# Optimization experiments

Hardware: AMD Instinct MI355X
Metric: run time of the kernel (lower is better)

Reference implementation:

```python
import jax, jax.numpy as jnp
import numpy as np

DIM = 768
N_HEADS = 12
HEAD_DIM = DIM // N_HEADS
BATCH = 2
SEQ = 4096


def setup_inputs() -> dict:
    key = jax.random.key(0)
    ks = jax.random.split(key, 9)
    s = 1.0 / np.sqrt(DIM)
    return {
        "x": jax.random.normal(ks[0], (BATCH, SEQ, DIM), dtype=jnp.float32),
        "Wq": jax.random.normal(ks[1], (DIM, DIM), dtype=jnp.float32) * s,
        "bq": jax.random.normal(ks[2], (DIM,), dtype=jnp.float32) * s,
        "Wk": jax.random.normal(ks[3], (DIM, DIM), dtype=jnp.float32) * s,
        "bk": jax.random.normal(ks[4], (DIM,), dtype=jnp.float32) * s,
        "Wv": jax.random.normal(ks[5], (DIM, DIM), dtype=jnp.float32) * s,
        "bv": jax.random.normal(ks[6], (DIM,), dtype=jnp.float32) * s,
        "Wo": jax.random.normal(ks[7], (DIM, DIM), dtype=jnp.float32) * s,
        "bo": jax.random.normal(ks[8], (DIM,), dtype=jnp.float32) * s,
    }


def reference(x, Wq, bq, Wk, bk, Wv, bv, Wo, bo):
    B, S, D = x.shape
    scale = 1.0 / np.sqrt(HEAD_DIM).astype(np.float32)
    # projections: [B,S,D] -> [B,H,S,Hd]
    def split_heads(t):
        return t.reshape(B, S, N_HEADS, HEAD_DIM).transpose(0, 2, 1, 3)
    q = split_heads(x @ Wq + bq)
    k = split_heads(x @ Wk + bk)
    v = split_heads(x @ Wv + bv)
    # full score matrix [B,H,S,S] as in the original (memory-bound)
    scores = jnp.einsum("bhqd,bhkd->bhqk", q, k) * scale
    attn = jax.nn.softmax(scores, axis=-1)
    out = jnp.einsum("bhqk,bhkd->bhqd", attn, v)
    out = out.transpose(0, 2, 1, 3).reshape(B, S, D)
    return out @ Wo + bo
```

## Files before the change

kernel.cpp:

```cpp
#include <hip/hip_runtime.h>
#include <hip/hip_bf16.h>
#include <math.h>

#define D_MODEL 768
#define NH 12
#define HD 64
#define BATCH 2
#define SEQ 4096
#define NROWS (BATCH * SEQ)

#define QSCALE 0.18033688011112042f

typedef __attribute__((ext_vector_type(8))) short short8;
typedef __attribute__((ext_vector_type(4))) short short4v;
typedef __attribute__((ext_vector_type(4))) float f32x4;
typedef __attribute__((ext_vector_type(16))) float f32x16;
typedef __attribute__((ext_vector_type(4))) unsigned int uint4v;

__device__ inline unsigned short f2bf(float f) {
    __hip_bfloat16 h = __float2bfloat16(f);
    return *reinterpret_cast<unsigned short*>(&h);
}

__device__ __forceinline__ unsigned int cvtpk_bf16(float lo, float hi) {
    unsigned int d;
    asm("v_cvt_pk_bf16_f32 %0, %1, %2" : "=v"(d) : "v"(lo), "v"(hi));
    return d;
}

__device__ __forceinline__ short8 u4_as_s8(uint4v u) {
    return *reinterpret_cast<short8*>(&u);
}

__device__ __forceinline__ void async_ld16(const unsigned short* g, unsigned short* l) {
    __builtin_amdgcn_global_load_lds(
        (const __attribute__((address_space(1))) void*)g,
        (__attribute__((address_space(3))) void*)l, 16, 0, 0);
}

__global__ __launch_bounds__(256) void convert_x_k(
    const float* __restrict__ x, unsigned short* __restrict__ xb)
{
    size_t i = ((size_t)blockIdx.x * 256 + threadIdx.x) * 8;
    float4 a = *(const float4*)(x + i);
    float4 b = *(const float4*)(x + i + 4);
    short8 o;
    o[0] = (short)f2bf(a.x); o[1] = (short)f2bf(a.y);
    o[2] = (short)f2bf(a.z); o[3] = (short)f2bf(a.w);
    o[4] = (short)f2bf(b.x); o[5] = (short)f2bf(b.y);
    o[6] = (short)f2bf(b.z); o[7] = (short)f2bf(b.w);
    *(short8*)(xb + i) = o;
}

__global__ __launch_bounds__(256) void convert_wt_k(
    const float* __restrict__ Wq, const float* __restrict__ Wk,
    const float* __restrict__ Wv, const float* __restrict__ Wo,
    unsigned short* __restrict__ wt)
{
    const float* W = (blockIdx.z == 0) ? Wq : (blockIdx.z == 1) ? Wk
                   : (blockIdx.z == 2) ? Wv : Wo;
    unsigned short* dst = wt + (size_t)blockIdx.z * D_MODEL * D_MODEL;
    __shared__ float tile[64][65];
    const int k0 = blockIdx.x * 64, n0 = blockIdx.y * 64;
    const int t = threadIdx.x;
    const int r = t >> 2, seg = t & 3;
    const float* src = W + (size_t)(k0 + r) * D_MODEL + n0 + seg * 16;
    #pragma unroll
    for (int i = 0; i < 4; ++i) {
        float4 v = *(const float4*)(src + i * 4);
        tile[r][seg * 16 + i * 4 + 0] = v.x;
        tile[r][seg * 16 + i * 4 + 1] = v.y;
        tile[r][seg * 16 + i * 4 + 2] = v.z;
        tile[r][seg * 16 + i * 4 + 3] = v.w;
    }
    __syncthreads();
    unsigned short* d = dst + (size_t)(n0 + r) * D_MODEL + k0 + seg * 16;
    short8 o0, o1;
    #pragma unroll
    for (int j = 0; j < 8; ++j) o0[j] = (short)f2bf(tile[seg * 16 + j][r]);
    #pragma unroll
    for (int j = 0; j < 8; ++j) o1[j] = (short)f2bf(tile[seg * 16 + 8 + j][r]);
    *(short8*)(d) = o0;
    *(short8*)(d + 8) = o1;
}

#define GEMM_STAGE(AS, BS, APTR, BPTR, KK)                                   \
    {                                                                        \
        _Pragma("unroll")                                                    \
        for (int j = 0; j < 4; ++j) {                                        \
            int c = (w * 4 + j) * 64 + lane;                                 \
            async_ld16(APTR + (size_t)(r0 + (c >> 3)) * D_MODEL + (KK) + (c & 7) * 8, \
                       &AS[0][0] + (size_t)c * 8);                           \
        }                                                                    \
        _Pragma("unroll")                                                    \
        for (int j = 0; j < 2; ++j) {                                        \
            int c = (w * 2 + j) * 64 + lane;                                 \
            async_ld16(BPTR + (size_t)(c0 + (c >> 3)) * D_MODEL + (KK) + (c & 7) * 8, \
                       &BS[0][0] + (size_t)c * 8);                           \
        }                                                                    \
    }

#define GEMM_COMPUTE(AS, BS)                                                 \
    {                                                                        \
        _Pragma("unroll")                                                    \
        for (int ks = 0; ks < 2; ++ks) {                                     \
            short8 af[2], bf[4];                                             \
            af[0] = *(const short8*)&AS[w * 32 + col][ks * 32 + quad * 8];   \
            af[1] = *(const short8*)&AS[w * 32 + 16 + col][ks * 32 + quad * 8]; \
            _Pragma("unroll")                                                \
            for (int nt = 0; nt < 4; ++nt)                                   \
                bf[nt] = *(const short8*)&BS[nt * 16 + col][ks * 32 + quad * 8]; \
            _Pragma("unroll")                                                \
            for (int mt = 0; mt < 2; ++mt)                                   \
                _Pragma("unroll")                                            \
                for (int nt = 0; nt < 4; ++nt)                               \
                    acc[mt][nt] = __builtin_amdgcn_mfma_f32_16x16x32_bf16(   \
                        af[mt], bf[nt], acc[mt][nt], 0, 0, 0);               \
        }                                                                    \
    }

__global__ __launch_bounds__(256) void qkv_mfma_k(
    const unsigned short* __restrict__ xb,
    const unsigned short* __restrict__ wt,
    const float* __restrict__ bq, const float* __restrict__ bk,
    const float* __restrict__ bv,
    unsigned short* __restrict__ qb,
    unsigned short* __restrict__ kb,
    unsigned short* __restrict__ vtb)
{
    __shared__ unsigned short As0[128][64], As1[128][64];
    __shared__ unsigned short Bs0[64][64],  Bs1[64][64];
    const int z = blockIdx.z;
    const unsigned short* Wt = wt + (size_t)z * D_MODEL * D_MODEL;
    const float* bias = (z == 0) ? bq : (z == 1) ? bk : bv;
    const int t = threadIdx.x;
    const int w = t >> 6, lane = t & 63, quad = lane >> 4, col = lane & 15;
    const int r0 = blockIdx.x * 128;
    const int c0 = blockIdx.y * 64;

    f32x4 acc[2][4] = {};

    GEMM_STAGE(As0, Bs0, xb, Wt, 0);
    __syncthreads();
    #pragma unroll
    for (int kp = 0; kp < 6; ++kp) {
        GEMM_STAGE(As1, Bs1, xb, Wt, kp * 128 + 64);
        GEMM_COMPUTE(As0, Bs0);
        __syncthreads();
        if (kp < 5) GEMM_STAGE(As0, Bs0, xb, Wt, kp * 128 + 128);
        GEMM_COMPUTE(As1, Bs1);
        __syncthreads();
    }

    const int h = blockIdx.y;
    #pragma unroll
    for (int nt = 0; nt < 4; ++nt) {
        const float bv_ = bias[c0 + nt * 16 + col];
        const int hd = nt * 16 + col;
        #pragma unroll
        for (int mt = 0; mt < 2; ++mt) {
            #pragma unroll
            for (int reg = 0; reg < 4; ++reg) {
                int r = r0 + w * 32 + mt * 16 + quad * 4 + reg;
                int b = r >> 12, s = r & (SEQ - 1);
                float val = acc[mt][nt][reg] + bv_;
                size_t bh = (size_t)(b * NH + h);
                if (z == 0)
                    qb[(bh * SEQ + s) * HD + hd] = f2bf(val * QSCALE);
                else if (z == 1)
                    kb[(bh * SEQ + s) * HD + hd] = f2bf(val);
                else
                    vtb[(bh * HD + hd) * SEQ + s] = f2bf(val);
            }
        }
    }
}

__global__ __launch_bounds__(256) void out_mfma_k(
    const unsigned short* __restrict__ ab,
    const unsigned short* __restrict__ wot,
    const float* __restrict__ bo,
    float* __restrict__ out)
{
    __shared__ unsigned short As0[128][64], As1[128][64];
    __shared__ unsigned short Bs0[64][64],  Bs1[64][64];
    const int t = threadIdx.x;
    const int w = t >> 6, lane = t & 63, quad = lane >> 4, col = lane & 15;
    const int r0 = blockIdx.x * 128;
    const int c0 = blockIdx.y * 64;

    f32x4 acc[2][4] = {};

    GEMM_STAGE(As0, Bs0, ab, wot, 0);
    __syncthreads();
    #pragma unroll
    for (int kp = 0; kp < 6; ++kp) {
        GEMM_STAGE(As1, Bs1, ab, wot, kp * 128 + 64);
        GEMM_COMPUTE(As0, Bs0);
        __syncthreads();
        if (kp < 5) GEMM_STAGE(As0, Bs0, ab, wot, kp * 128 + 128);
        GEMM_COMPUTE(As1, Bs1);
        __syncthreads();
    }

    #pragma unroll
    for (int nt = 0; nt < 4; ++nt) {
        const float bv_ = bo[c0 + nt * 16 + col];
        #pragma unroll
        for (int mt = 0; mt < 2; ++mt) {
            #pragma unroll
            for (int reg = 0; reg < 4; ++reg) {
                int r = r0 + w * 32 + mt * 16 + quad * 4 + reg;
                out[(size_t)r * D_MODEL + c0 + nt * 16 + col] = acc[mt][nt][reg] + bv_;
            }
        }
    }
}

__device__ __forceinline__ void softmax_pack(
    const f32x16& s, float& lsum, short8& pf0, short8& pf1)
{
    float p[16];
    #pragma unroll
    for (int r = 0; r < 16; ++r)
        p[r] = __builtin_amdgcn_exp2f(s[r]);
    lsum += (((p[0] + p[1]) + (p[2] + p[3])) + ((p[4] + p[5]) + (p[6] + p[7])))
          + (((p[8] + p[9]) + (p[10] + p[11])) + ((p[12] + p[13]) + (p[14] + p[15])));
    unsigned int c01 = cvtpk_bf16(p[0],  p[1]);
    unsigned int c45 = cvtpk_bf16(p[4],  p[5]);
    unsigned int c23 = cvtpk_bf16(p[2],  p[3]);
    unsigned int c67 = cvtpk_bf16(p[6],  p[7]);
    unsigned int c89 = cvtpk_bf16(p[8],  p[9]);
    unsigned int cCD = cvtpk_bf16(p[12], p[13]);
    unsigned int cAB = cvtpk_bf16(p[10], p[11]);
    unsigned int cEF = cvtpk_bf16(p[14], p[15]);
    auto r0 = __builtin_amdgcn_permlane32_swap((int)c01, (int)c45, false, false);
    auto r1 = __builtin_amdgcn_permlane32_swap((int)c23, (int)c67, false, false);
    auto r2 = __builtin_amdgcn_permlane32_swap((int)c89, (int)cCD, false, false);
    auto r3 = __builtin_amdgcn_permlane32_swap((int)cAB, (int)cEF, false, false);
    uint4v u0, u1;
    u0[0] = (unsigned int)r0[0]; u0[1] = (unsigned int)r1[0];
    u0[2] = (unsigned int)r0[1]; u0[3] = (unsigned int)r1[1];
    u1[0] = (unsigned int)r2[0]; u1[1] = (unsigned int)r3[0];
    u1[2] = (unsigned int)r2[1]; u1[3] = (unsigned int)r3[1];
    pf0 = u4_as_s8(u0);
    pf1 = u4_as_s8(u1);
}

__global__ __launch_bounds__(256) void flash_mfma_k(
    const unsigned short* __restrict__ qb,
    const unsigned short* __restrict__ kb,
    const unsigned short* __restrict__ vtb,
    unsigned short* __restrict__ ab)
{
    __shared__ unsigned short Ks[64][66];
    __shared__ unsigned short Vts[64][66];

    const int t = threadIdx.x;
    const int w = t >> 6, lane = t & 63;
    const int l31 = lane & 31, hi = lane >> 5;
    const int q0 = blockIdx.x * 128;
    const int h = blockIdx.y, b = blockIdx.z;
    const size_t bh = (size_t)b * NH + h;
    const unsigned short* qg = qb + bh * SEQ * HD;
    const unsigned short* kg = kb + bh * SEQ * HD;
    const unsigned short* vg = vtb + bh * HD * SEQ;

    short8 qf[4];
    {
        const unsigned short* src = qg + (size_t)(q0 + w * 32 + l31) * HD + hi * 8;
        #pragma unroll
        for (int ks = 0; ks < 4; ++ks)
            qf[ks] = *(const short8*)(src + ks * 16);
    }

    f32x16 oacc[2] = {};
    float lsum = 0.f;
    const int srow = lane, sseg = w;

    short8 kr0, kr1, vr0, vr1;
    {
        const unsigned short* kp = kg + (size_t)srow * HD + sseg * 16;
        kr0 = *(const short8*)(kp);
        kr1 = *(const short8*)(kp + 8);
        const unsigned short* vp = vg + (size_t)srow * SEQ + sseg * 16;
        vr0 = *(const short8*)(vp);
        vr1 = *(const short8*)(vp + 8);
    }

    for (int kt = 0; kt < SEQ; kt += 64) {
        __syncthreads();
        *(short8*)&Ks[srow][sseg * 16]      = kr0;
        *(short8*)&Ks[srow][sseg * 16 + 8]  = kr1;
        *(short8*)&Vts[srow][sseg * 16]     = vr0;
        *(short8*)&Vts[srow][sseg * 16 + 8] = vr1;
        if (kt + 64 < SEQ) {
            const unsigned short* kp = kg + (size_t)(kt + 64 + srow) * HD + sseg * 16;
            kr0 = *(const short8*)(kp);
            kr1 = *(const short8*)(kp + 8);
            const unsigned short* vp = vg + (size_t)srow * SEQ + kt + 64 + sseg * 16;
            vr0 = *(const short8*)(vp);
            vr1 = *(const short8*)(vp + 8);
        }
        __syncthreads();

        short8 pf[4];
        #pragma unroll
        for (int kti = 0; kti < 2; ++kti) {
            f32x16 s = {};
            __builtin_amdgcn_s_setprio(1);
            #pragma unroll
            for (int ks = 0; ks < 4; ++ks) {
                short8 kf = *(const short8*)&Ks[kti * 32 + l31][ks * 16 + hi * 8];
                s = __builtin_amdgcn_mfma_f32_32x32x16_bf16(kf, qf[ks], s, 0, 0, 0);
            }
            __builtin_amdgcn_s_setprio(0);
            softmax_pack(s, lsum, pf[kti * 2 + 0], pf[kti * 2 + 1]);
        }

        __builtin_amdgcn_s_setprio(1);
        #pragma unroll
        for (int ks = 0; ks < 4; ++ks) {
            short8 pfk = pf[ks];
            #pragma unroll
            for (int dt = 0; dt < 2; ++dt) {
                short8 vf = *(const short8*)&Vts[dt * 32 + l31][ks * 16 + hi * 8];
                oacc[dt] = __builtin_amdgcn_mfma_f32_32x32x16_bf16(
                    vf, pfk, oacc[dt], 0, 0, 0);
            }
        }
        __builtin_amdgcn_s_setprio(0);
    }

    lsum += __shfl_xor(lsum, 32);
    float inv = 1.0f / lsum;
    int s = q0 + w * 32 + l31;
    unsigned short* dst = ab + ((size_t)b * SEQ + s) * D_MODEL + h * HD;
    #pragma unroll
    for (int dt = 0; dt < 2; ++dt) {
        #pragma unroll
        for (int rq = 0; rq < 4; ++rq) {
            short4v o4;
            o4[0] = (short)f2bf(oacc[dt][rq * 4 + 0] * inv);
            o4[1] = (short)f2bf(oacc[dt][rq * 4 + 1] * inv);
            o4[2] = (short)f2bf(oacc[dt][rq * 4 + 2] * inv);
            o4[3] = (short)f2bf(oacc[dt][rq * 4 + 3] * inv);
            *(short4v*)(dst + dt * 32 + rq * 8 + hi * 4) = o4;
        }
    }
}

extern "C" void kernel_launch(void* const* d_in, const int* in_sizes, int n_in,
                              void* d_out, int out_size, void* d_ws, size_t ws_size,
                              hipStream_t stream)
{
    const float* x  = (const float*)d_in[0];
    const float* Wq = (const float*)d_in[1];
    const float* bq = (const float*)d_in[2];
    const float* Wk = (const float*)d_in[3];
    const float* bk = (const float*)d_in[4];
    const float* Wv = (const float*)d_in[5];
    const float* bv = (const float*)d_in[6];
    const float* Wo = (const float*)d_in[7];
    const float* bo = (const float*)d_in[8];
    float* out = (float*)d_out;

    const size_t n_x  = (size_t)NROWS * D_MODEL;
    const size_t n_w  = (size_t)D_MODEL * D_MODEL;
    unsigned short* xb  = (unsigned short*)d_ws;
    unsigned short* wt  = xb + n_x;
    unsigned short* qb  = wt + 4 * n_w;
    unsigned short* kb  = qb + n_x;
    unsigned short* vtb = kb + n_x;
    unsigned short* ab  = vtb + n_x;
    const size_t need = ((size_t)5 * n_x + 4 * n_w) * sizeof(unsigned short);
    if (ws_size < need) return;

    convert_x_k<<<dim3((int)(n_x / 2048)), 256, 0, stream>>>(x, xb);
    convert_wt_k<<<dim3(12, 12, 4), 256, 0, stream>>>(Wq, Wk, Wv, Wo, wt);
    qkv_mfma_k<<<dim3(NROWS / 128, D_MODEL / 64, 3), 256, 0, stream>>>(
        xb, wt, bq, bk, bv, qb, kb, vtb);
    flash_mfma_k<<<dim3(SEQ / 128, NH, BATCH), 256, 0, stream>>>(qb, kb, vtb, ab);
    out_mfma_k<<<dim3(NROWS / 128, D_MODEL / 64), 256, 0, stream>>>(
        ab, wt + 3 * n_w, bo, out);
}
```

Measured before the change: 295.6 us.

## Fuse Q/K/V projections into one kernel sharing the x tile

Replaces the three-way z-dimension QKV GEMM launch with a single kernel in which each block loads one x tile and multiplies it against all three weight slices, keeping three accumulator sets. This removes the repeated loading of x for Q, K and V. In exchange the double-buffered async pipeline is dropped in favour of a single-buffered loop with two barriers per k-step. Register use also triples and the grid shrinks to a third of its size, which may reduce latency hiding.

```diff
diff --git a/kernel.cpp b/kernel.cpp
--- a/kernel.cpp
+++ b/kernel.cpp
@@ -82,6 +82,92 @@
     for (int j = 0; j < 8; ++j) o1[j] = (short)f2bf(tile[seg * 16 + 8 + j][r]);
     *(short8*)(d) = o0;
     *(short8*)(d + 8) = o1;
+}
+
+__global__ __launch_bounds__(256, 3) void qkv_fused_k(
+    const unsigned short* __restrict__ xb,
+    const unsigned short* __restrict__ wt,
+    const float* __restrict__ bq, const float* __restrict__ bk,
+    const float* __restrict__ bv,
+    unsigned short* __restrict__ qb,
+    unsigned short* __restrict__ kb,
+    unsigned short* __restrict__ vtb)
+{
+    __shared__ unsigned short As[128][64];
+    __shared__ unsigned short Bs[3][64][64];
+    const int t = threadIdx.x;
+    const int w = t >> 6, lane = t & 63, quad = lane >> 4, col = lane & 15;
+    const int r0 = blockIdx.x * 128;
+    const int c0 = blockIdx.y * 64;
+
+    f32x4 acc[3][2][4] = {};
+
+    for (int kk = 0; kk < D_MODEL; kk += 64) {
+        __syncthreads();
+        #pragma unroll
+        for (int j = 0; j < 4; ++j) {
+            int c = (w * 4 + j) * 64 + lane;
+            async_ld16(xb + (size_t)(r0 + (c >> 3)) * D_MODEL + kk + (c & 7) * 8,
+                       &As[0][0] + (size_t)c * 8);
+        }
+        #pragma unroll
+        for (int z = 0; z < 3; ++z) {
+            const unsigned short* Wt = wt + (size_t)z * D_MODEL * D_MODEL;
+            #pragma unroll
+            for (int j = 0; j < 2; ++j) {
+                int c = (w * 2 + j) * 64 + lane;
+                async_ld16(Wt + (size_t)(c0 + (c >> 3)) * D_MODEL + kk + (c & 7) * 8,
+                           &Bs[z][0][0] + (size_t)c * 8);
+            }
+        }
+        __syncthreads();
+        #pragma unroll
+        for (int ks = 0; ks < 2; ++ks) {
+            short8 af[2];
+            af[0] = *(const short8*)&As[w * 32 + col][ks * 32 + quad * 8];
+            af[1] = *(const short8*)&As[w * 32 + 16 + col][ks * 32 + quad * 8];
+            #pragma unroll
+            for (int z = 0; z < 3; ++z) {
+                short8 bf[4];
+                #pragma unroll
+                for (int nt = 0; nt < 4; ++nt)
+                    bf[nt] = *(const short8*)&Bs[z][nt * 16 + col][ks * 32 + quad * 8];
+                #pragma unroll
+                for (int mt = 0; mt < 2; ++mt)
+                    #pragma unroll
+                    for (int nt = 0; nt < 4; ++nt)
+                        acc[z][mt][nt] = __builtin_amdgcn_mfma_f32_16x16x32_bf16(
+                            af[mt], bf[nt], acc[z][mt][nt], 0, 0, 0);
+            }
+        }
+    }
+
+    const int h = blockIdx.y;
+    #pragma unroll
+    for (int z = 0; z < 3; ++z) {
+        const float* bias = (z == 0) ? bq : (z == 1) ? bk : bv;
+        #pragma unroll
+        for (int nt = 0; nt < 4; ++nt) {
+            const float bv_ = bias[c0 + nt * 16 + col];
+            const int hd = nt * 16 + col;
+            #pragma unroll
+            for (int mt = 0; mt < 2; ++mt) {
+                #pragma unroll
+                for (int reg = 0; reg < 4; ++reg) {
+                    int r = r0 + w * 32 + mt * 16 + quad * 4 + reg;
+                    int b = r >> 12, s = r & (SEQ - 1);
+                    float val = acc[z][mt][nt][reg] + bv_;
+                    size_t bh = (size_t)(b * NH + h);
+                    if (z == 0)
+                        qb[(bh * SEQ + s) * HD + hd] = f2bf(val * QSCALE);
+                    else if (z == 1)
+                        kb[(bh * SEQ + s) * HD + hd] = f2bf(val);
+                    else
+                        vtb[(bh * HD + hd) * SEQ + s] = f2bf(val);
+                }
+            }
+        }
+    }
 }
 
 #define GEMM_STAGE(AS, BS, APTR, BPTR, KK)                                   \
@@ -118,63 +204,6 @@
                         af[mt], bf[nt], acc[mt][nt], 0, 0, 0);               \
         }                                                                    \
     }
-
-__global__ __launch_bounds__(256) void qkv_mfma_k(
-    const unsigned short* __restrict__ xb,
-    const unsigned short* __restrict__ wt,
-    const float* __restrict__ bq, const float* __restrict__ bk,
-    const float* __restrict__ bv,
-    unsigned short* __restrict__ qb,
-    unsigned short* __restrict__ kb,
-    unsigned short* __restrict__ vtb)
-{
-    __shared__ unsigned short As0[128][64], As1[128][64];
-    __shared__ unsigned short Bs0[64][64],  Bs1[64][64];
-    const int z = blockIdx.z;
-    const unsigned short* Wt = wt + (size_t)z * D_MODEL * D_MODEL;
-    const float* bias = (z == 0) ? bq : (z == 1) ? bk : bv;
-    const int t = threadIdx.x;
-    const int w = t >> 6, lane = t & 63, quad = lane >> 4, col = lane & 15;
-    const int r0 = blockIdx.x * 128;
-    const int c0 = blockIdx.y * 64;
-
-    f32x4 acc[2][4] = {};
-
-    GEMM_STAGE(As0, Bs0, xb, Wt, 0);
-    __syncthreads();
-    #pragma unroll
-    for (int kp = 0; kp < 6; ++kp) {
-        GEMM_STAGE(As1, Bs1, xb, Wt, kp * 128 + 64);
-        GEMM_COMPUTE(As0, Bs0);
-        __syncthreads();
-        if (kp < 5) GEMM_STAGE(As0, Bs0, xb, Wt, kp * 128 + 128);
-        GEMM_COMPUTE(As1, Bs1);
-        __syncthreads();
-    }
-
-    const int h = blockIdx.y;
-    #pragma unroll
-    for (int nt = 0; nt < 4; ++nt) {
-        const float bv_ = bias[c0 + nt * 16 + col];
-        const int hd = nt * 16 + col;
-        #pragma unroll
-        for (int mt = 0; mt < 2; ++mt) {
-            #pragma unroll
-            for (int reg = 0; reg < 4; ++reg) {
-                int r = r0 + w * 32 + mt * 16 + quad * 4 + reg;
-                int b = r >> 12, s = r & (SEQ - 1);
-                float val = acc[mt][nt][reg] + bv_;
-                size_t bh = (size_t)(b * NH + h);
-                if (z == 0)
-                    qb[(bh * SEQ + s) * HD + hd] = f2bf(val * QSCALE);
-                else if (z == 1)
-                    kb[(bh * SEQ + s) * HD + hd] = f2bf(val);
-                else
-                    vtb[(bh * HD + hd) * SEQ + s] = f2bf(val);
-            }
-        }
-    }
-}
 
 __global__ __launch_bounds__(256) void out_mfma_k(
     const unsigned short* __restrict__ ab,
@@ -378,7 +407,7 @@
 
     convert_x_k<<<dim3((int)(n_x / 2048)), 256, 0, stream>>>(x, xb);
     convert_wt_k<<<dim3(12, 12, 4), 256, 0, stream>>>(Wq, Wk, Wv, Wo, wt);
-    qkv_mfma_k<<<dim3(NROWS / 128, D_MODEL / 64, 3), 256, 0, stream>>>(
+    qkv_fused_k<<<dim3(NROWS / 128, D_MODEL / 64), 256, 0, stream>>>(
         xb, wt, bq, bk, bv, qb, kb, vtb);
     flash_mfma_k<<<dim3(SEQ / 128, NH, BATCH), 256, 0, stream>>>(qb, kb, vtb, ab);
     out_mfma_k<<<dim3(NROWS / 128, D_MODEL / 64), 256, 0, stream>>>(
```

Result: faster. 281.5 us (-4.8%).
